# Optimization experiments

Hardware: AMD Instinct MI355X
Metric: run time of the kernel (lower is better)

## Reference

```python
import math
import jax, jax.numpy as jnp
import numpy as np

S = 64.0
M = 0.5
C = 1.5
K = 16
EPS = 1e-6
IN = 128
OUT = 10000
B = 1024


def _l2norm(x, axis):
    # matches torch.nn.functional.normalize (eps=1e-12)
    n = jnp.linalg.norm(x, axis=axis, keepdims=True)
    return x / jnp.maximum(n, 1e-12)


def setup_inputs() -> dict:
    key = jax.random.key(0)
    k1, k2, k3, k4 = jax.random.split(key, 4)
    inp = jax.random.normal(k1, (B, IN), dtype=jnp.float32)
    factor = jax.random.uniform(k2, (B, 1), dtype=jnp.float32)
    label = jax.random.randint(k3, (B,), 0, OUT)
    # xavier_uniform over (k, in, out): fan_in=IN, fan_out=OUT (last two dims)
    limit = math.sqrt(6.0 / (IN + OUT))
    weight = jax.random.uniform(k4, (K, IN, OUT), dtype=jnp.float32, minval=-limit, maxval=limit)
    return {"input": inp, "factor": factor, "label": label, "weight": weight}


def reference(input, factor, label, weight):
    # disguise-adaptive margin: (B,1)
    func_a = jnp.power(C, factor / 12.0) * M
    threshold = math.pi - func_a  # (B,1)

    xn = _l2norm(input, axis=1)          # (B, IN)
    wn = _l2norm(weight, axis=1)         # (K, IN, OUT), normalized along IN

    # batched sub-center matmul then max over sub-centers k
    cos_all = jnp.einsum('bf,kfo->kbo', xn, wn)   # (K, B, OUT)
    cos_theta = jnp.max(cos_all, axis=0)          # (B, OUT)

    theta = jnp.arccos(jnp.clip(cos_theta, -1.0 + EPS, 1.0 - EPS))
    one_hot = jax.nn.one_hot(label, OUT, dtype=theta.dtype)  # (B, OUT)
    selected = jnp.where(theta > threshold, jnp.zeros_like(one_hot), one_hot)
    logits = jnp.cos(jnp.where(selected.astype(bool), theta + func_a, theta)) * S

    # cross-entropy (mean reduction)
    logp = jax.nn.log_softmax(logits, axis=-1)
    cls_loss = -jnp.mean(jnp.take_along_axis(logp, label[:, None], axis=1))

    # top-1 accuracy (percent), detached stat
    pred = jnp.argmax(logits, axis=1)
    prec1 = jnp.mean((pred == label).astype(jnp.float32)) * 100.0
    return cls_loss, prec1
```

## Files before the change

### kernel.cpp

```cpp
#include <hip/hip_runtime.h>
#include <hip/hip_bf16.h>
#include <math.h>

#define BB    1024
#define FIN   128
#define NOUT  10000
#define NBLK  79
#define NCB   158
#define NK    16
#define NPART (NCB * 2)
#define LDX   136

typedef __attribute__((ext_vector_type(8))) short short8;
typedef __attribute__((ext_vector_type(4))) float floatx4;

__device__ __forceinline__ unsigned packbf(float a, float b) {
    __hip_bfloat162 h = __float22bfloat162_rn(make_float2(a, b));
    union { __hip_bfloat162 h2; unsigned u; } v;
    v.h2 = h;
    return v.u;
}

__device__ __forceinline__ unsigned scale2(unsigned p, float wi) {
    float lo = __uint_as_float(p << 16) * wi;
    float hi = __uint_as_float(p & 0xffff0000u) * wi;
    return packbf(lo, hi);
}

__device__ __forceinline__ void async16(const void* g, void* l) {
    __builtin_amdgcn_global_load_lds(
        (const __attribute__((address_space(1))) unsigned int*)g,
        (__attribute__((address_space(3))) unsigned int*)l, 16, 0, 0);
}

__global__ void rowprep(const float* __restrict__ X, const float* __restrict__ factor,
                        float* __restrict__ xinv, float* __restrict__ fa_out,
                        float* __restrict__ thr_out) {
    int b = blockIdx.x;
    int lane = threadIdx.x;
    float v0 = X[b * FIN + lane];
    float v1 = X[b * FIN + 64 + lane];
    float s = v0 * v0 + v1 * v1;
    #pragma unroll
    for (int off = 32; off > 0; off >>= 1) s += __shfl_down(s, off);
    if (lane == 0) {
        xinv[b] = 1.0f / fmaxf(sqrtf(s), 1e-12f);
        float fa = powf(1.5f, factor[b] * (1.0f / 12.0f)) * 0.5f;
        fa_out[b] = fa;
        thr_out[b] = (float)M_PI - fa;
    }
}

__global__ __launch_bounds__(256) void wconv(
    const float* __restrict__ W, unsigned char* __restrict__ Wbf,
    const float* __restrict__ X, const float* __restrict__ factor,
    float* __restrict__ xinv, float* __restrict__ fa_out, float* __restrict__ thr_out) {

    __shared__ float s[64 * 64];
    __shared__ uint4 wout[1024];
    __shared__ float sq2[256];
    __shared__ float wis[64];

    const int tid = threadIdx.x;

    if (blockIdx.x >= NK * NCB) {
        int rb = blockIdx.x - NK * NCB;
        int w4 = tid >> 6, lane = tid & 63;
        for (int i = w4; i < 64; i += 4) {
            int row = rb * 64 + i;
            float v0 = X[row * FIN + lane];
            float v1 = X[row * FIN + 64 + lane];
            float ss = v0 * v0 + v1 * v1;
            #pragma unroll
            for (int off = 32; off > 0; off >>= 1) ss += __shfl_down(ss, off);
            if (lane == 0) {
                xinv[row] = 1.0f / fmaxf(sqrtf(ss), 1e-12f);
                float fa = powf(1.5f, factor[row] * (1.0f / 12.0f)) * 0.5f;
                fa_out[row] = fa;
                thr_out[row] = (float)M_PI - fa;
            }
        }
        return;
    }

    const int k  = blockIdx.x / NCB;
    const int cb = blockIdx.x - k * NCB;
    const int o0 = cb * 64;
    const int col = tid & 63, seg = tid >> 6;
    const int c   = tid >> 2, sub = tid & 3;
    const int wn_ = c >> 5, n2_ = (c >> 4) & 1, l15_ = c & 15;

    float sqacc = 0.0f;
    #pragma unroll
    for (int h = 0; h < 2; h++) {
        #pragma unroll
        for (int it = 0; it < 4; it++) {
            int idx = it * 256 + tid;
            int f = idx >> 4, c4 = idx & 15;
            int o = o0 + c4 * 4;
            float4 v = make_float4(0.f, 0.f, 0.f, 0.f);
            if (o < NOUT)
                v = *(const float4*)(W + (size_t)(k * FIN + h * 64 + f) * NOUT + o);
            *(float4*)(s + f * 64 + c4 * 4) = v;
        }
        __syncthreads();
        float ss = 0.0f;
        #pragma unroll
        for (int f2 = 0; f2 < 16; f2++) {
            float x = s[(seg * 16 + f2) * 64 + col];
            ss = fmaf(x, x, ss);
        }
        sqacc += ss;
        #pragma unroll
        for (int i = 0; i < 2; i++) {
            int tcl = sub * 2 + i;
            int tcg = h * 8 + tcl;
            int kk = tcg >> 2, qq = tcg & 3;
            int fb = tcl * 8;
            uint4 u;
            u.x = packbf(s[(fb + 0) * 64 + c], s[(fb + 1) * 64 + c]);
            u.y = packbf(s[(fb + 2) * 64 + c], s[(fb + 3) * 64 + c]);
            u.z = packbf(s[(fb + 4) * 64 + c], s[(fb + 5) * 64 + c]);
            u.w = packbf(s[(fb + 6) * 64 + c], s[(fb + 7) * 64 + c]);
            wout[wn_ * 512 + n2_ * 256 + kk * 64 + qq * 16 + l15_] = u;
        }
        __syncthreads();
    }
    sq2[tid] = sqacc;
    __syncthreads();
    if (tid < 64)
        wis[tid] = 1.0f / fmaxf(sqrtf(sq2[tid] + sq2[tid + 64] + sq2[tid + 128] + sq2[tid + 192]), 1e-12f);
    __syncthreads();

    unsigned char* dst = Wbf + ((size_t)k * NCB + cb) * 16384;
    #pragma unroll
    for (int i = 0; i < 4; i++) {
        int idx = i * 256 + tid;
        int ccol = ((idx >> 9) << 5) + (((idx >> 8) & 1) << 4) + (idx & 15);
        float wi = wis[ccol];
        uint4 u = wout[idx];
        uint4 r;
        r.x = scale2(u.x, wi);
        r.y = scale2(u.y, wi);
        r.z = scale2(u.z, wi);
        r.w = scale2(u.w, wi);
        *(uint4*)(dst + (size_t)idx * 16) = r;
    }
}

__global__ __launch_bounds__(512, 2) void gemm_mx(
    const float* __restrict__ X, const unsigned char* __restrict__ Wbf,
    const int* __restrict__ label, const float* __restrict__ xinv,
    float2* __restrict__ partial, float* __restrict__ cosl) {

    __shared__ union {
        short xs[128 * LDX];
        short bb[3][8192];
    } u;

    const int tid  = threadIdx.x;
    const int lane = tid & 63;
    const int w    = tid >> 6;
    const int l15  = lane & 15;
    const int q    = lane >> 4;
    const int wm   = w & 3;
    const int wn   = w >> 2;

    const int id    = blockIdx.x;
    const int group = id >> 6;
    const int sub   = id & 63;
    const int cb    = group * 8 + (sub & 7);
    const int y     = sub >> 3;
    if (cb >= NCB) return;
    const int r0 = y * 128;
    const int o0 = cb * 64;

    #pragma unroll
    for (int it = 0; it < 8; it++) {
        int idx = it * 512 + tid;
        int row = idx >> 5;
        int c4  = idx & 31;
        const float4 v = *(const float4*)(X + (size_t)(r0 + row) * FIN + c4 * 4);
        float xi = xinv[r0 + row];
        uint2 p;
        p.x = packbf(v.x * xi, v.y * xi);
        p.y = packbf(v.z * xi, v.w * xi);
        *(uint2*)(u.xs + row * LDX + c4 * 4) = p;
    }
    __syncthreads();

    short8 af[2][4];
    #pragma unroll
    for (int mt = 0; mt < 2; mt++)
        #pragma unroll
        for (int kk = 0; kk < 4; kk++)
            af[mt][kk] = *(const short8*)(u.xs + (wm * 32 + mt * 16 + l15) * LDX + kk * 32 + q * 8);
    __syncthreads();

    auto issue = [&](int k, short* d) {
        const unsigned char* g = Wbf + ((size_t)k * NCB + cb) * 16384
                                 + (size_t)w * 2048 + (size_t)lane * 16;
        short* dw = d + w * 1024;
        async16(g, dw);
        async16(g + 1024, dw + 512);
    };

    short* rd = u.bb[0];
    short* nx = u.bb[1];
    short* wr = u.bb[2];

    issue(0, rd);
    issue(1, nx);

    floatx4 maxv[2][2];
    #pragma unroll
    for (int mt = 0; mt < 2; mt++)
        #pragma unroll
        for (int n2 = 0; n2 < 2; n2++)
            #pragma unroll
            for (int r = 0; r < 4; r++)
                maxv[mt][n2][r] = -INFINITY;

    for (int k = 0; k < NK; k++) {
        if (k == NK - 1) {
            asm volatile("s_waitcnt vmcnt(0)" ::: "memory");
        } else {
            asm volatile("s_waitcnt vmcnt(2)" ::: "memory");
        }
        __builtin_amdgcn_s_barrier();
        if (k < NK - 2) issue(k + 2, wr);

        const short* wt = rd;

        floatx4 acc[2][2];
        #pragma unroll
        for (int mt = 0; mt < 2; mt++)
            #pragma unroll
            for (int n2 = 0; n2 < 2; n2++)
                acc[mt][n2] = (floatx4){0.f, 0.f, 0.f, 0.f};
        #pragma unroll
        for (int kk = 0; kk < 4; kk++) {
            short8 bf[2];
            #pragma unroll
            for (int n2 = 0; n2 < 2; n2++)
                bf[n2] = *(const short8*)(wt + wn * 4096 + n2 * 2048 + kk * 512 + lane * 8);
            #pragma unroll
            for (int mt = 0; mt < 2; mt++)
                #pragma unroll
                for (int n2 = 0; n2 < 2; n2++)
                    acc[mt][n2] = __builtin_amdgcn_mfma_f32_16x16x32_bf16(
                        af[mt][kk], bf[n2], acc[mt][n2], 0, 0, 0);
        }
        #pragma unroll
        for (int mt = 0; mt < 2; mt++)
            #pragma unroll
            for (int n2 = 0; n2 < 2; n2++)
                #pragma unroll
                for (int r = 0; r < 4; r++)
                    maxv[mt][n2][r] = fmaxf(maxv[mt][n2][r], acc[mt][n2][r]);

        short* t = rd; rd = nx; nx = wr; wr = t;
    }

    #pragma unroll
    for (int mt = 0; mt < 2; mt++) {
        #pragma unroll
        for (int rr = 0; rr < 4; rr++) {
            int row = r0 + wm * 32 + mt * 16 + q * 4 + rr;
            int lb = label[row];
            float m = -1e30f, sum = 0.f;
            #pragma unroll
            for (int n2 = 0; n2 < 2; n2++) {
                int o = o0 + wn * 32 + n2 * 16 + l15;
                if (o < NOUT) {
                    float cc = maxv[mt][n2][rr];
                    if (o == lb) {
                        cosl[row] = cc;
                    } else {
                        float l = 64.0f * fminf(fmaxf(cc, -1.0f + 1e-6f), 1.0f - 1e-6f);
                        sum += __expf(l - 64.0f);
                        m = fmaxf(m, l);
                    }
                }
            }
            #pragma unroll
            for (int off = 1; off <= 8; off <<= 1) {
                sum += __shfl_xor(sum, off);
                m = fmaxf(m, __shfl_xor(m, off));
            }
            if (l15 == 0)
                partial[(size_t)row * NPART + cb * 2 + wn] = make_float2(m, sum);
        }
    }
}

__global__ __launch_bounds__(256, 2) void gemm_stats(
    const float* __restrict__ X, const float* __restrict__ W,
    const int* __restrict__ label, const float* __restrict__ xinv,
    float2* __restrict__ partial, float* __restrict__ cosl) {

    __shared__ short xs[128 * LDX];
    __shared__ short wt[128 * LDX];
    __shared__ float sqs[128][2];

    const int tid  = threadIdx.x;
    const int lane = tid & 63;
    const int w    = tid >> 6;
    const int l15  = lane & 15;
    const int q    = lane >> 4;
    const int wm   = w & 1;
    const int wn   = w >> 1;

    const int id    = blockIdx.x;
    const int group = id >> 6;
    const int sub   = id & 63;
    const int jb    = group * 8 + (sub & 7);
    const int y     = sub >> 3;
    if (jb >= NBLK) return;
    const int r0 = y * 128;
    const int o0 = jb * 128;

    #pragma unroll
    for (int it = 0; it < 16; it++) {
        int idx = it * 256 + tid;
        int row = idx >> 5;
        int c4  = idx & 31;
        const float4 v = *(const float4*)(X + (size_t)(r0 + row) * FIN + c4 * 4);
        uint2 p;
        p.x = packbf(v.x, v.y);
        p.y = packbf(v.z, v.w);
        *(uint2*)(xs + row * LDX + c4 * 4) = p;
    }

    const int st_o = (w & 1) * 64 + lane;
    const int st_f = (w >> 1) * 64;
    const int st_h = w >> 1;
    const int go   = o0 + st_o;
    const bool ov  = go < NOUT;

    float rw[64];
    {
        const float* Wp = W + (size_t)st_f * NOUT + go;
        #pragma unroll
        for (int g = 0; g < 16; g++)
            #pragma unroll
            for (int cc = 0; cc < 4; cc++)
                rw[g * 4 + cc] = ov ? Wp[(size_t)(g * 4 + cc) * NOUT] : 0.0f;
    }
    __syncthreads();

    short8 af[4][4];
    #pragma unroll
    for (int mt = 0; mt < 4; mt++)
        #pragma unroll
        for (int kk = 0; kk < 4; kk++)
            af[mt][kk] = *(const short8*)(xs + (wm * 64 + mt * 16 + l15) * LDX + kk * 32 + q * 8);

    floatx4 maxv[4][4];
    #pragma unroll
    for (int mt = 0; mt < 4; mt++)
        #pragma unroll
        for (int nt = 0; nt < 4; nt++)
            #pragma unroll
            for (int r = 0; r < 4; r++)
                maxv[mt][nt][r] = -INFINITY;

    for (int k = 0; k < NK; k++) {
        float sq = 0.0f;
        uint2 pk[16];
        #pragma unroll
        for (int g = 0; g < 16; g++) {
            float a0 = rw[g * 4 + 0], a1 = rw[g * 4 + 1];
            float a2 = rw[g * 4 + 2], a3 = rw[g * 4 + 3];
            sq = fmaf(a0, a0, sq); sq = fmaf(a1, a1, sq);
            sq = fmaf(a2, a2, sq); sq = fmaf(a3, a3, sq);
            pk[g].x = packbf(a0, a1);
            pk[g].y = packbf(a2, a3);
        }
        __syncthreads();
        #pragma unroll
        for (int g = 0; g < 16; g++)
            *(uint2*)(wt + st_o * LDX + st_f + g * 4) = pk[g];
        sqs[st_o][st_h] = sq;
        __syncthreads();

        if (k < NK - 1) {
            const float* Wn = W + ((size_t)(k + 1) * FIN + st_f) * NOUT + go;
            #pragma unroll
            for (int g = 0; g < 16; g++)
                #pragma unroll
                for (int cc = 0; cc < 4; cc++)
                    rw[g * 4 + cc] = ov ? Wn[(size_t)(g * 4 + cc) * NOUT] : 0.0f;
        }

        float wv[4];
        #pragma unroll
        for (int nt = 0; nt < 4; nt++) {
            int colx = wn * 64 + nt * 16 + l15;
            wv[nt] = 1.0f / fmaxf(sqrtf(sqs[colx][0] + sqs[colx][1]), 1e-12f);
        }

        #pragma unroll
        for (int h = 0; h < 2; h++) {
            floatx4 acc[4][2];
            #pragma unroll
            for (int mt = 0; mt < 4; mt++) {
                acc[mt][0] = (floatx4){0.f, 0.f, 0.f, 0.f};
                acc[mt][1] = (floatx4){0.f, 0.f, 0.f, 0.f};
            }
            #pragma unroll
            for (int kk = 0; kk < 4; kk++) {
                short8 bf0 = *(const short8*)(wt + (wn * 64 + (h * 2 + 0) * 16 + l15) * LDX + kk * 32 + q * 8);
                short8 bf1 = *(const short8*)(wt + (wn * 64 + (h * 2 + 1) * 16 + l15) * LDX + kk * 32 + q * 8);
                #pragma unroll
                for (int mt = 0; mt < 4; mt++) {
                    acc[mt][0] = __builtin_amdgcn_mfma_f32_16x16x32_bf16(af[mt][kk], bf0, acc[mt][0], 0, 0, 0);
                    acc[mt][1] = __builtin_amdgcn_mfma_f32_16x16x32_bf16(af[mt][kk], bf1, acc[mt][1], 0, 0, 0);
                }
            }
            #pragma unroll
            for (int mt = 0; mt < 4; mt++)
                #pragma unroll
                for (int n2 = 0; n2 < 2; n2++)
                    #pragma unroll
                    for (int r = 0; r < 4; r++)
                        maxv[mt][h * 2 + n2][r] =
                            fmaxf(maxv[mt][h * 2 + n2][r], acc[mt][n2][r] * wv[h * 2 + n2]);
        }
    }

    #pragma unroll
    for (int mt = 0; mt < 4; mt++) {
        #pragma unroll
        for (int rr = 0; rr < 4; rr++) {
            int row = r0 + wm * 64 + mt * 16 + q * 4 + rr;
            float xi = xinv[row];
            int lb = label[row];
            float m = -1e30f, sum = 0.f;
            #pragma unroll
            for (int nt = 0; nt < 4; nt++) {
                int o = o0 + wn * 64 + nt * 16 + l15;
                if (o < NOUT) {
                    float cc = maxv[mt][nt][rr] * xi;
                    if (o == lb) {
                        cosl[row] = cc;
                    } else {
                        float l = 64.0f * fminf(fmaxf(cc, -1.0f + 1e-6f), 1.0f - 1e-6f);
                        sum += __expf(l - 64.0f);
                        m = fmaxf(m, l);
                    }
                }
            }
            #pragma unroll
            for (int off = 1; off <= 8; off <<= 1) {
                sum += __shfl_xor(sum, off);
                m = fmaxf(m, __shfl_xor(m, off));
            }
            if (l15 == 0) {
                partial[(size_t)row * NPART + jb * 4 + wn * 2 + 0] = make_float2(m, sum);
                partial[(size_t)row * NPART + jb * 4 + wn * 2 + 1] = make_float2(-1e30f, 0.f);
            }
        }
    }
}

__global__ void finalize_rows(const float2* __restrict__ partial, const float* __restrict__ cosl,
                              const float* __restrict__ fa, const float* __restrict__ thr,
                              float2* __restrict__ rowres, int np) {
    int w = threadIdx.x >> 6;
    int lane = threadIdx.x & 63;
    int b = blockIdx.x * 4 + w;
    float m = -1e30f, s = 0.0f;
    for (int j = lane; j < np; j += 64) {
        float2 p = partial[(size_t)b * np + j];
        s += p.y;
        m = fmaxf(m, p.x);
    }
    #pragma unroll
    for (int off = 1; off < 64; off <<= 1) {
        s += __shfl_xor(s, off);
        m = fmaxf(m, __shfl_xor(m, off));
    }
    if (lane == 0) {
        float c = fminf(fmaxf(cosl[b], -1.0f + 1e-6f), 1.0f - 1e-6f);
        float theta = acosf(c);
        float ll = (theta > thr[b]) ? 64.0f * c : 64.0f * cosf(theta + fa[b]);
        float S = s + __expf(ll - 64.0f);
        float loss = 64.0f + logf(S) - ll;
        rowres[b] = make_float2(loss, (ll > m) ? 100.0f : 0.0f);
    }
}

__global__ void finalize_sum(const float2* __restrict__ rowres, float* __restrict__ out) {
    __shared__ float sl[1024];
    __shared__ float sc[1024];
    int b = threadIdx.x;
    float2 v = rowres[b];
    sl[b] = v.x;
    sc[b] = v.y;
    __syncthreads();
    for (int st = 512; st > 0; st >>= 1) {
        if (b < st) { sl[b] += sl[b + st]; sc[b] += sc[b + st]; }
        __syncthreads();
    }
    if (b == 0) {
        out[0] = sl[0] * (1.0f / 1024.0f);
        out[1] = sc[0] * (1.0f / 1024.0f);
    }
}

extern "C" void kernel_launch(void* const* d_in, const int* in_sizes, int n_in,
                              void* d_out, int out_size, void* d_ws, size_t ws_size,
                              hipStream_t stream) {
    const float* X      = (const float*)d_in[0];
    const float* factor = (const float*)d_in[1];
    const int*   label  = (const int*)d_in[2];
    const float* W      = (const float*)d_in[3];
    float* out = (float*)d_out;
    float* ws  = (float*)d_ws;

    float*  xinv = ws;
    float*  fa   = ws + 1024;
    float*  thr  = ws + 2048;
    float*  cosl = ws + 3072;
    float2* rowres = (float2*)(ws + 4096);
    float2* partial = (float2*)(ws + 6144);
    unsigned char* Wbf = (unsigned char*)d_ws + 4 * 1024 * 1024;

    const size_t wbf_bytes = (size_t)NK * NCB * 16384;
    const size_t need = 4ull * 1024 * 1024 + wbf_bytes;

    if (ws_size >= need) {
        wconv<<<NK * NCB + 16, 256, 0, stream>>>(W, Wbf, X, factor, xinv, fa, thr);
        gemm_mx<<<1280, 512, 0, stream>>>(X, Wbf, label, xinv, partial, cosl);
    } else {
        rowprep<<<BB, 64, 0, stream>>>(X, factor, xinv, fa, thr);
        gemm_stats<<<640, 256, 0, stream>>>(X, W, label, xinv, partial, cosl);
    }
    finalize_rows<<<BB / 4, 256, 0, stream>>>(partial, cosl, fa, thr, rowres, NPART);
    finalize_sum<<<1, BB, 0, stream>>>(rowres, out);
}
```

Before: 205.5 us.

## Reshape gemm_mx warp tiling to 64x16 and merge per-block partial stats in LDS

Changes the warp layout in gemm_mx from a 4x2 grid with 32x32 tiles to a 2x4 grid with 64x16 tiles. Each warp now loads one B fragment per k-step and reuses it across four A tiles, which cuts LDS reads of the weight tile at the cost of more A-fragment registers. It also combines the four per-warp (max, sum) partials for each row through shared memory, so each block writes one partial instead of two. This halves the partial array that finalize_rows must read, but adds two block-wide barriers at the end.

```diff
diff --git a/kernel.cpp b/kernel.cpp
--- a/kernel.cpp
+++ b/kernel.cpp
@@ -9,6 +9,7 @@
 #define NCB   158
 #define NK    16
 #define NPART (NCB * 2)
+#define NPARTM NCB
 #define LDX   136
 
 typedef __attribute__((ext_vector_type(8))) short short8;
@@ -156,6 +157,7 @@
     __shared__ union {
         short xs[128 * LDX];
         short bb[3][8192];
+        float2 ms[128][4];
     } u;
 
     const int tid  = threadIdx.x;
@@ -163,8 +165,8 @@
     const int w    = tid >> 6;
     const int l15  = lane & 15;
     const int q    = lane >> 4;
-    const int wm   = w & 3;
-    const int wn   = w >> 2;
+    const int wm   = w & 1;
+    const int wn   = w >> 1;
 
     const int id    = blockIdx.x;
     const int group = id >> 6;
@@ -189,12 +191,12 @@
     }
     __syncthreads();
 
-    short8 af[2][4];
-    #pragma unroll
-    for (int mt = 0; mt < 2; mt++)
+    short8 af[4][4];
+    #pragma unroll
+    for (int mt = 0; mt < 4; mt++)
         #pragma unroll
         for (int kk = 0; kk < 4; kk++)
-            af[mt][kk] = *(const short8*)(u.xs + (wm * 32 + mt * 16 + l15) * LDX + kk * 32 + q * 8);
+            af[mt][kk] = *(const short8*)(u.xs + (wm * 64 + mt * 16 + l15) * LDX + kk * 32 + q * 8);
     __syncthreads();
 
     auto issue = [&](int k, short* d) {
@@ -212,14 +214,14 @@
     issue(0, rd);
     issue(1, nx);
 
-    floatx4 maxv[2][2];
-    #pragma unroll
-    for (int mt = 0; mt < 2; mt++)
-        #pragma unroll
-        for (int n2 = 0; n2 < 2; n2++)
-            #pragma unroll
-            for (int r = 0; r < 4; r++)
-                maxv[mt][n2][r] = -INFINITY;
+    floatx4 maxv[4];
+    #pragma unroll
+    for (int mt = 0; mt < 4; mt++)
+        #pragma unroll
+        for (int r = 0; r < 4; r++)
+            maxv[mt][r] = -INFINITY;
+
+    const int wboff = wn * 2048 + lane * 8;
 
     for (int k = 0; k < NK; k++) {
         if (k == NK - 1) {
@@ -230,57 +232,48 @@
         __builtin_amdgcn_s_barrier();
         if (k < NK - 2) issue(k + 2, wr);
 
-        const short* wt = rd;
-
-        floatx4 acc[2][2];
-        #pragma unroll
-        for (int mt = 0; mt < 2; mt++)
-            #pragma unroll
-            for (int n2 = 0; n2 < 2; n2++)
-                acc[mt][n2] = (floatx4){0.f, 0.f, 0.f, 0.f};
+        const short* wt = rd + wboff;
+
+        floatx4 acc[4];
+        #pragma unroll
+        for (int mt = 0; mt < 4; mt++)
+            acc[mt] = (floatx4){0.f, 0.f, 0.f, 0.f};
         #pragma unroll
         for (int kk = 0; kk < 4; kk++) {
-            short8 bf[2];
-            #pragma unroll
-            for (int n2 = 0; n2 < 2; n2++)
-                bf[n2] = *(const short8*)(wt + wn * 4096 + n2 * 2048 + kk * 512 + lane * 8);
-            #pragma unroll
-            for (int mt = 0; mt < 2; mt++)
-                #pragma unroll
-                for (int n2 = 0; n2 < 2; n2++)
-                    acc[mt][n2] = __builtin_amdgcn_mfma_f32_16x16x32_bf16(
-                        af[mt][kk], bf[n2], acc[mt][n2], 0, 0, 0);
-        }
-        #pragma unroll
-        for (int mt = 0; mt < 2; mt++)
-            #pragma unroll
-            for (int n2 = 0; n2 < 2; n2++)
-                #pragma unroll
-                for (int r = 0; r < 4; r++)
-                    maxv[mt][n2][r] = fmaxf(maxv[mt][n2][r], acc[mt][n2][r]);
+            short8 bf = *(const short8*)(wt + kk * 512);
+            #pragma unroll
+            for (int mt = 0; mt < 4; mt++)
+                acc[mt] = __builtin_amdgcn_mfma_f32_16x16x32_bf16(
+                    af[mt][kk], bf, acc[mt], 0, 0, 0);
+        }
+        #pragma unroll
+        for (int mt = 0; mt < 4; mt++)
+            #pragma unroll
+            for (int r = 0; r < 4; r++)
+                maxv[mt][r] = fmaxf(maxv[mt][r], acc[mt][r]);
 
         short* t = rd; rd = nx; nx = wr; wr = t;
     }
 
-    #pragma unroll
-    for (int mt = 0; mt < 2; mt++) {
+    __syncthreads();
+
+    #pragma unroll
+    for (int mt = 0; mt < 4; mt++) {
         #pragma unroll
         for (int rr = 0; rr < 4; rr++) {
-            int row = r0 + wm * 32 + mt * 16 + q * 4 + rr;
+            int rloc = wm * 64 + mt * 16 + q * 4 + rr;
+            int row = r0 + rloc;
             int lb = label[row];
             float m = -1e30f, sum = 0.f;
-            #pragma unroll
-            for (int n2 = 0; n2 < 2; n2++) {
-                int o = o0 + wn * 32 + n2 * 16 + l15;
-                if (o < NOUT) {
-                    float cc = maxv[mt][n2][rr];
-                    if (o == lb) {
-                        cosl[row] = cc;
-                    } else {
-                        float l = 64.0f * fminf(fmaxf(cc, -1.0f + 1e-6f), 1.0f - 1e-6f);
-                        sum += __expf(l - 64.0f);
-                        m = fmaxf(m, l);
-                    }
+            int o = o0 + wn * 16 + l15;
+            if (o < NOUT) {
+                float cc = maxv[mt][rr];
+                if (o == lb) {
+                    cosl[row] = cc;
+                } else {
+                    float l = 64.0f * fminf(fmaxf(cc, -1.0f + 1e-6f), 1.0f - 1e-6f);
+                    sum = __expf(l - 64.0f);
+                    m = l;
                 }
             }
             #pragma unroll
@@ -289,8 +282,17 @@
                 m = fmaxf(m, __shfl_xor(m, off));
             }
             if (l15 == 0)
-                partial[(size_t)row * NPART + cb * 2 + wn] = make_float2(m, sum);
-        }
+                u.ms[rloc][wn] = make_float2(m, sum);
+        }
+    }
+    __syncthreads();
+
+    if (tid < 128) {
+        float2 a = u.ms[tid][0], b = u.ms[tid][1];
+        float2 c2 = u.ms[tid][2], d = u.ms[tid][3];
+        float m = fmaxf(fmaxf(a.x, b.x), fmaxf(c2.x, d.x));
+        float s = (a.y + b.y) + (c2.y + d.y);
+        partial[(size_t)(r0 + tid) * NPARTM + cb] = make_float2(m, s);
     }
 }
 
@@ -533,10 +535,11 @@
     if (ws_size >= need) {
         wconv<<<NK * NCB + 16, 256, 0, stream>>>(W, Wbf, X, factor, xinv, fa, thr);
         gemm_mx<<<1280, 512, 0, stream>>>(X, Wbf, label, xinv, partial, cosl);
+        finalize_rows<<<BB / 4, 256, 0, stream>>>(partial, cosl, fa, thr, rowres, NPARTM);
     } else {
         rowprep<<<BB, 64, 0, stream>>>(X, factor, xinv, fa, thr);
         gemm_stats<<<640, 256, 0, stream>>>(X, W, label, xinv, partial, cosl);
-    }
-    finalize_rows<<<BB / 4, 256, 0, stream>>>(partial, cosl, fa, thr, rowres, NPART);
+        finalize_rows<<<BB / 4, 256, 0, stream>>>(partial, cosl, fa, thr, rowres, NPART);
+    }
     finalize_sum<<<1, BB, 0, stream>>>(rowres, out);
 }
```

Measured after the change: 281.7 us. 37.1% more time.
